# Performance work log

Measured on AMD Instinct MI355X. Metric: run time of the kernel, lower is better.

Reference implementation:

```python
import jax, jax.numpy as jnp
import numpy as np
from jax import lax

B, T, L = 128, 512, 256


def setup_inputs() -> dict:
    key = jax.random.key(0)
    k1, k2, k3 = jax.random.split(key, 3)
    labels = jax.random.randint(k1, (B, T), 0, L)
    y_true = jax.nn.one_hot(labels, L, dtype=jnp.float32)  # (B, T, L) one-hot
    y_pre = jax.random.normal(k2, (B, T, L), dtype=jnp.float32)
    trans = jax.random.normal(k3, (L, L), dtype=jnp.float32) * 0.1
    return {"y_true": y_true, "y_pre": y_pre, "trans": trans}


def reference(y_true, y_pre, trans):
    # path score: emission part + transition part
    point_score = jnp.sum(y_pre * y_true, axis=(1, 2))[:, None]  # (B, 1)
    # sum_t  one_hot(y_t)^T @ trans @ one_hot(y_{t+1})
    trans_score = jnp.einsum('btl,lm,btm->b', y_true[:, :-1], trans, y_true[:, 1:])[:, None]
    path_score = point_score + trans_score  # (B, 1)

    # forward algorithm (log-space DP) over timesteps
    def step(state, emit):
        # state: (B, L) log alpha, emit: (B, L) emissions at current step
        scores = state[:, :, None] + trans[None, :, :] + emit[:, None, :]  # (B, L, L)
        new = jax.nn.logsumexp(scores, axis=1)  # (B, L)
        return new, None

    init = y_pre[:, 0]                         # (B, L)
    emits = jnp.moveaxis(y_pre[:, 1:], 1, 0)   # (T-1, B, L)
    final, _ = lax.scan(step, init, emits)
    log_norm = jax.nn.logsumexp(final, axis=1, keepdims=True)  # (B, 1)
    return log_norm - path_score
```

## Files before the change

### kernel.cpp

```cpp
#include <hip/hip_runtime.h>
#include <hip/hip_bf16.h>

#define B_ 128
#define T_ 512
#define L_ 256

typedef float f32x4 __attribute__((ext_vector_type(4)));
typedef unsigned uint32x4 __attribute__((ext_vector_type(4)));

__device__ __forceinline__ unsigned short f2bf(float x) {
    unsigned u = __builtin_bit_cast(unsigned, x);
    return (unsigned short)((u + 0x7fff + ((u >> 16) & 1)) >> 16);
}

#define AW(n, v) asm volatile("v_accvgpr_write_b32 a" #n ", %0" :: "v"(v) : "a" #n)
#define STGF(F, A0, A1, A2, A3) { uint32x4 qq = etb4[vbase + F * 64]; \
    AW(A0, qq[0]); AW(A1, qq[1]); AW(A2, qq[2]); AW(A3, qq[3]); }

#define MFMA_AB(ACC, AF, LO, HI) \
    asm volatile("v_mfma_f32_16x16x32_bf16 %0, %1, a[" #LO ":" #HI "], %0" \
                 : "+v"(ACC) : "v"(AF))

#define BARRIER() asm volatile("s_waitcnt lgkmcnt(0)\n\ts_barrier" ::: "memory")

__global__ __launch_bounds__(256) void k_exptrans(const float* __restrict__ trans,
                                                  unsigned short* __restrict__ ETB) {
    int l = blockIdx.x;
    int m = threadIdx.x;
    unsigned short v = f2bf(__expf(trans[l * L_ + m]));
    unsigned byte = (unsigned)((m >> 4) * 8 + (l >> 5)) * 1024u
                  + (unsigned)(((l >> 3) & 3) * 16 + (m & 15)) * 16u
                  + (unsigned)(((l >> 1) & 3)) * 4u + (unsigned)(l & 1) * 2u;
    *(unsigned short*)((char*)ETB + byte) = v;
}

__global__ __launch_bounds__(256) void k_labels(const float* __restrict__ y_true,
                                                int* __restrict__ labels) {
    int wid = threadIdx.x >> 6, lane = threadIdx.x & 63;
    int r = blockIdx.x * 4 + wid;
    const float4* row = (const float4*)(y_true + (size_t)r * L_);
    float4 v = row[lane];
    int loc = -1;
    if (v.x > 0.5f) loc = lane * 4 + 0;
    if (v.y > 0.5f) loc = lane * 4 + 1;
    if (v.z > 0.5f) loc = lane * 4 + 2;
    if (v.w > 0.5f) loc = lane * 4 + 3;
    unsigned long long m = __ballot(loc >= 0);
    int src = __ffsll(m) - 1;
    int lab = __shfl(loc, src, 64);
    if (lane == 0) labels[r] = lab;
}

__global__ __launch_bounds__(256) void k_path(const float* __restrict__ y_pre,
                                              const float* __restrict__ trans,
                                              const int* __restrict__ labels,
                                              float* __restrict__ path) {
    int b = blockIdx.x, tid = threadIdx.x;
    const int* lb = labels + b * T_;
    float acc = 0.f;
    for (int t = tid; t < T_; t += 256) {
        int l1 = lb[t];
        acc += y_pre[((size_t)b * T_ + t) * L_ + l1];
        if (t + 1 < T_) acc += trans[l1 * L_ + lb[t + 1]];
    }
#pragma unroll
    for (int off = 1; off < 64; off <<= 1) acc += __shfl_xor(acc, off, 64);
    __shared__ float red[4];
    int wid = tid >> 6, lane = tid & 63;
    if (lane == 0) red[wid] = acc;
    __syncthreads();
    if (tid == 0) path[b] = red[0] + red[1] + red[2] + red[3];
}

#define MFMA32()                                                         \
        MFMA_AB(c0, af0,   0,   3); MFMA_AB(c1, af0,  32,  35);          \
        MFMA_AB(c2, af0,  64,  67); MFMA_AB(c3, af0,  96,  99);          \
        MFMA_AB(c0, af1,   4,   7); MFMA_AB(c1, af1,  36,  39);          \
        MFMA_AB(c2, af1,  68,  71); MFMA_AB(c3, af1, 100, 103);          \
        MFMA_AB(c0, af2,   8,  11); MFMA_AB(c1, af2,  40,  43);          \
        MFMA_AB(c2, af2,  72,  75); MFMA_AB(c3, af2, 104, 107);          \
        MFMA_AB(c0, af3,  12,  15); MFMA_AB(c1, af3,  44,  47);          \
        MFMA_AB(c2, af3,  76,  79); MFMA_AB(c3, af3, 108, 111);          \
        MFMA_AB(c0, af4,  16,  19); MFMA_AB(c1, af4,  48,  51);          \
        MFMA_AB(c2, af4,  80,  83); MFMA_AB(c3, af4, 112, 115);          \
        MFMA_AB(c0, af5,  20,  23); MFMA_AB(c1, af5,  52,  55);          \
        MFMA_AB(c2, af5,  84,  87); MFMA_AB(c3, af5, 116, 119);          \
        MFMA_AB(c0, af6,  24,  27); MFMA_AB(c1, af6,  56,  59);          \
        MFMA_AB(c2, af6,  88,  91); MFMA_AB(c3, af6, 120, 123);          \
        MFMA_AB(c0, af7,  28,  31); MFMA_AB(c1, af7,  60,  63);          \
        MFMA_AB(c2, af7,  92,  95); MFMA_AB(c3, af7, 124, 127);

#define STEP(TT, PH_RD, PH_WR, DSLOT, WSLOT, EREG)                       \
    {                                                                    \
        float Dt = nmr[DSLOT];               \
        float scale = __expf(NPprev + EREG - Dt);   \
        const uint32x4* pA = (const uint32x4*)ph[PH_RD];                 \
        uint32x4 af0 = pA[g];      uint32x4 af1 = pA[g + 4];             \
        uint32x4 af2 = pA[g + 8];  uint32x4 af3 = pA[g + 12];            \
        uint32x4 af4 = pA[g + 16]; uint32x4 af5 = pA[g + 20];            \
        uint32x4 af6 = pA[g + 24]; uint32x4 af7 = pA[g + 28];            \
        f32x4 c0 = {0.f,0.f,0.f,0.f}, c1 = {0.f,0.f,0.f,0.f};            \
        f32x4 c2 = {0.f,0.f,0.f,0.f}, c3 = {0.f,0.f,0.f,0.f};            \
        MFMA32()                                                         \
        float val = (g < 2) ? ((g == 0) ? c0[0] : c1[0])                 \
                            : ((g == 2) ? c2[0] : c3[0]);                \
        ph[PH_WR][st] = f2bf(val * scale);    \
        s = NPprev + __logf(val) + EREG;                 \
        if (tid == 0) nmr[WSLOT] = s;               \
        NPprev = Dt;                                                     \
        { int tp = (TT) + 4; if (tp > T_ - 1) tp = T_ - 1;               \
          EREG = yp[(size_t)tp * L_ + st]; }     \
        BARRIER();                                                       \
    }

__global__ void __launch_bounds__(256, 1)
k_forward(const float* __restrict__ yp_all,
          const unsigned short* __restrict__ ETB,
          const float* __restrict__ path,
          float* __restrict__ out) {
    int b = blockIdx.x, tid = threadIdx.x;
    int w = tid >> 6;
    int i = tid & 63;
    int g = i >> 4;
    const int st = (w << 6) + i;
    const float* yp = yp_all + (size_t)b * T_ * L_;

    {
        const uint32x4* etb4 = (const uint32x4*)ETB;
        int vbase = w * 2048 + i;
        STGF( 0,   0,  1,  2,  3)  STGF( 1,   4,  5,  6,  7)
        STGF( 2,   8,  9, 10, 11)  STGF( 3,  12, 13, 14, 15)
        STGF( 4,  16, 17, 18, 19)  STGF( 5,  20, 21, 22, 23)
        STGF( 6,  24, 25, 26, 27)  STGF( 7,  28, 29, 30, 31)
        STGF( 8,  32, 33, 34, 35)  STGF( 9,  36, 37, 38, 39)
        STGF(10,  40, 41, 42, 43)  STGF(11,  44, 45, 46, 47)
        STGF(12,  48, 49, 50, 51)  STGF(13,  52, 53, 54, 55)
        STGF(14,  56, 57, 58, 59)  STGF(15,  60, 61, 62, 63)
        STGF(16,  64, 65, 66, 67)  STGF(17,  68, 69, 70, 71)
        STGF(18,  72, 73, 74, 75)  STGF(19,  76, 77, 78, 79)
        STGF(20,  80, 81, 82, 83)  STGF(21,  84, 85, 86, 87)
        STGF(22,  88, 89, 90, 91)  STGF(23,  92, 93, 94, 95)
        STGF(24,  96, 97, 98, 99)  STGF(25, 100,101,102,103)
        STGF(26, 104,105,106,107)  STGF(27, 108,109,110,111)
        STGF(28, 112,113,114,115)  STGF(29, 116,117,118,119)
        STGF(30, 120,121,122,123)  STGF(31, 124,125,126,127)
    }

    __shared__ alignas(16) unsigned short ph[2][L_];
    __shared__ float red[8];
    __shared__ float nmr[4];

    float s = yp[st];
    {
        float v = s;
#pragma unroll
        for (int off = 1; off < 64; off <<= 1) v = fmaxf(v, __shfl_xor(v, off, 64));
        if (i == 0) red[w] = v;
        __syncthreads();
        if (tid == 0) {
            float M = fmaxf(fmaxf(red[0], red[1]), fmaxf(red[2], red[3]));
            nmr[0] = M; nmr[1] = M; nmr[2] = M; nmr[3] = M;
        }
        __syncthreads();
    }
    float NPprev = nmr[0];
    ph[1][st] = f2bf(__expf(s - NPprev));

    float e0 = yp[(size_t)1 * L_ + st];
    float e1 = yp[(size_t)2 * L_ + st];
    float e2 = yp[(size_t)3 * L_ + st];
    float e3 = yp[(size_t)4 * L_ + st];
    __syncthreads();

    for (int t = 1; t < 509; t += 4) {
        STEP(t + 0, 1, 0, 3, 1, e0)
        STEP(t + 1, 0, 1, 0, 2, e1)
        STEP(t + 2, 1, 0, 1, 3, e2)
        STEP(t + 3, 0, 1, 2, 0, e3)
    }
    STEP(509, 1, 0, 3, 1, e0)
    STEP(510, 0, 1, 0, 2, e1)
    STEP(511, 1, 0, 1, 3, e2)

    {
        float v = s;
#pragma unroll
        for (int off = 1; off < 64; off <<= 1) v = fmaxf(v, __shfl_xor(v, off, 64));
        if (i == 0) red[w] = v;
    }
    __syncthreads();
    float M = fmaxf(fmaxf(red[0], red[1]), fmaxf(red[2], red[3]));
    float e = __expf(s - M);
#pragma unroll
    for (int off = 1; off < 64; off <<= 1) e += __shfl_xor(e, off, 64);
    if (i == 0) red[4 + w] = e;
    __syncthreads();
    if (tid == 0)
        out[b] = M + __logf((red[4] + red[5]) + (red[6] + red[7])) - path[b];
}

extern "C" void kernel_launch(void* const* d_in, const int* in_sizes, int n_in,
                              void* d_out, int out_size, void* d_ws, size_t ws_size,
                              hipStream_t stream) {
    const float* y_true = (const float*)d_in[0];
    const float* y_pre  = (const float*)d_in[1];
    const float* trans  = (const float*)d_in[2];
    float* out = (float*)d_out;

    char* ws = (char*)d_ws;
    unsigned short* ETB = (unsigned short*)ws;
    int* labels = (int*)(ws + 131072);
    float* path = (float*)(ws + 131072 + 262144);

    hipLaunchKernelGGL(k_exptrans, dim3(L_), dim3(L_), 0, stream, trans, ETB);
    hipLaunchKernelGGL(k_labels, dim3(B_ * T_ / 4), dim3(256), 0, stream, y_true, labels);
    hipLaunchKernelGGL(k_path, dim3(B_), dim3(256), 0, stream, y_pre, trans, labels, path);
    hipLaunchKernelGGL(k_forward, dim3(B_), dim3(256), 0, stream, y_pre, ETB, path, out);
}
```

Measured before the change: 243.9 us.

## Process two batch sequences per block to interleave independent forward recurrences

Each forward block now runs the log-space DP for two batch elements at once. The two independent MFMA chains are interleaved so their latencies overlap, and both share one barrier and one transposed-exp(trans) register preload per step. This cuts the grid from 128 to 64 blocks, which uses fewer CUs on a 256-CU part, and doubles per-thread register and LDS work. The emission prefetch depth drops from four steps ahead to two.

```diff
diff --git a/kernel.cpp b/kernel.cpp
--- a/kernel.cpp
+++ b/kernel.cpp
@@ -72,44 +72,74 @@
     if (tid == 0) path[b] = red[0] + red[1] + red[2] + red[3];
 }
 
-#define MFMA32()                                                         \
-        MFMA_AB(c0, af0,   0,   3); MFMA_AB(c1, af0,  32,  35);          \
-        MFMA_AB(c2, af0,  64,  67); MFMA_AB(c3, af0,  96,  99);          \
-        MFMA_AB(c0, af1,   4,   7); MFMA_AB(c1, af1,  36,  39);          \
-        MFMA_AB(c2, af1,  68,  71); MFMA_AB(c3, af1, 100, 103);          \
-        MFMA_AB(c0, af2,   8,  11); MFMA_AB(c1, af2,  40,  43);          \
-        MFMA_AB(c2, af2,  72,  75); MFMA_AB(c3, af2, 104, 107);          \
-        MFMA_AB(c0, af3,  12,  15); MFMA_AB(c1, af3,  44,  47);          \
-        MFMA_AB(c2, af3,  76,  79); MFMA_AB(c3, af3, 108, 111);          \
-        MFMA_AB(c0, af4,  16,  19); MFMA_AB(c1, af4,  48,  51);          \
-        MFMA_AB(c2, af4,  80,  83); MFMA_AB(c3, af4, 112, 115);          \
-        MFMA_AB(c0, af5,  20,  23); MFMA_AB(c1, af5,  52,  55);          \
-        MFMA_AB(c2, af5,  84,  87); MFMA_AB(c3, af5, 116, 119);          \
-        MFMA_AB(c0, af6,  24,  27); MFMA_AB(c1, af6,  56,  59);          \
-        MFMA_AB(c2, af6,  88,  91); MFMA_AB(c3, af6, 120, 123);          \
-        MFMA_AB(c0, af7,  28,  31); MFMA_AB(c1, af7,  60,  63);          \
-        MFMA_AB(c2, af7,  92,  95); MFMA_AB(c3, af7, 124, 127);
-
-#define STEP(TT, PH_RD, PH_WR, DSLOT, WSLOT, EREG)                       \
+#define MFMA64()                                                         \
+    MFMA_AB(cA0, aA0,   0,   3); MFMA_AB(cB0, aB0,   0,   3);            \
+    MFMA_AB(cA1, aA0,  32,  35); MFMA_AB(cB1, aB0,  32,  35);            \
+    MFMA_AB(cA2, aA0,  64,  67); MFMA_AB(cB2, aB0,  64,  67);            \
+    MFMA_AB(cA3, aA0,  96,  99); MFMA_AB(cB3, aB0,  96,  99);            \
+    MFMA_AB(cA0, aA1,   4,   7); MFMA_AB(cB0, aB1,   4,   7);            \
+    MFMA_AB(cA1, aA1,  36,  39); MFMA_AB(cB1, aB1,  36,  39);            \
+    MFMA_AB(cA2, aA1,  68,  71); MFMA_AB(cB2, aB1,  68,  71);            \
+    MFMA_AB(cA3, aA1, 100, 103); MFMA_AB(cB3, aB1, 100, 103);            \
+    MFMA_AB(cA0, aA2,   8,  11); MFMA_AB(cB0, aB2,   8,  11);            \
+    MFMA_AB(cA1, aA2,  40,  43); MFMA_AB(cB1, aB2,  40,  43);            \
+    MFMA_AB(cA2, aA2,  72,  75); MFMA_AB(cB2, aB2,  72,  75);            \
+    MFMA_AB(cA3, aA2, 104, 107); MFMA_AB(cB3, aB2, 104, 107);            \
+    MFMA_AB(cA0, aA3,  12,  15); MFMA_AB(cB0, aB3,  12,  15);            \
+    MFMA_AB(cA1, aA3,  44,  47); MFMA_AB(cB1, aB3,  44,  47);            \
+    MFMA_AB(cA2, aA3,  76,  79); MFMA_AB(cB2, aB3,  76,  79);            \
+    MFMA_AB(cA3, aA3, 108, 111); MFMA_AB(cB3, aB3, 108, 111);            \
+    MFMA_AB(cA0, aA4,  16,  19); MFMA_AB(cB0, aB4,  16,  19);            \
+    MFMA_AB(cA1, aA4,  48,  51); MFMA_AB(cB1, aB4,  48,  51);            \
+    MFMA_AB(cA2, aA4,  80,  83); MFMA_AB(cB2, aB4,  80,  83);            \
+    MFMA_AB(cA3, aA4, 112, 115); MFMA_AB(cB3, aB4, 112, 115);            \
+    MFMA_AB(cA0, aA5,  20,  23); MFMA_AB(cB0, aB5,  20,  23);            \
+    MFMA_AB(cA1, aA5,  52,  55); MFMA_AB(cB1, aB5,  52,  55);            \
+    MFMA_AB(cA2, aA5,  84,  87); MFMA_AB(cB2, aB5,  84,  87);            \
+    MFMA_AB(cA3, aA5, 116, 119); MFMA_AB(cB3, aB5, 116, 119);            \
+    MFMA_AB(cA0, aA6,  24,  27); MFMA_AB(cB0, aB6,  24,  27);            \
+    MFMA_AB(cA1, aA6,  56,  59); MFMA_AB(cB1, aB6,  56,  59);            \
+    MFMA_AB(cA2, aA6,  88,  91); MFMA_AB(cB2, aB6,  88,  91);            \
+    MFMA_AB(cA3, aA6, 120, 123); MFMA_AB(cB3, aB6, 120, 123);            \
+    MFMA_AB(cA0, aA7,  28,  31); MFMA_AB(cB0, aB7,  28,  31);            \
+    MFMA_AB(cA1, aA7,  60,  63); MFMA_AB(cB1, aB7,  60,  63);            \
+    MFMA_AB(cA2, aA7,  92,  95); MFMA_AB(cB2, aB7,  92,  95);            \
+    MFMA_AB(cA3, aA7, 124, 127); MFMA_AB(cB3, aB7, 124, 127);
+
+#define STEPD(TT, PH_RD, PH_WR, DSLOT, WSLOT, EA, EB)                    \
     {                                                                    \
-        float Dt = nmr[DSLOT];               \
-        float scale = __expf(NPprev + EREG - Dt);   \
-        const uint32x4* pA = (const uint32x4*)ph[PH_RD];                 \
-        uint32x4 af0 = pA[g];      uint32x4 af1 = pA[g + 4];             \
-        uint32x4 af2 = pA[g + 8];  uint32x4 af3 = pA[g + 12];            \
-        uint32x4 af4 = pA[g + 16]; uint32x4 af5 = pA[g + 20];            \
-        uint32x4 af6 = pA[g + 24]; uint32x4 af7 = pA[g + 28];            \
-        f32x4 c0 = {0.f,0.f,0.f,0.f}, c1 = {0.f,0.f,0.f,0.f};            \
-        f32x4 c2 = {0.f,0.f,0.f,0.f}, c3 = {0.f,0.f,0.f,0.f};            \
-        MFMA32()                                                         \
-        float val = (g < 2) ? ((g == 0) ? c0[0] : c1[0])                 \
-                            : ((g == 2) ? c2[0] : c3[0]);                \
-        ph[PH_WR][st] = f2bf(val * scale);    \
-        s = NPprev + __logf(val) + EREG;                 \
-        if (tid == 0) nmr[WSLOT] = s;               \
-        NPprev = Dt;                                                     \
-        { int tp = (TT) + 4; if (tp > T_ - 1) tp = T_ - 1;               \
-          EREG = yp[(size_t)tp * L_ + st]; }     \
+        float eAc = EA, eBc = EB;            \
+        { int tp = (TT) + 2; if (tp > T_ - 1) tp = T_ - 1;               \
+          EA = ypA[(size_t)tp * L_ + st];                                \
+          EB = ypB[(size_t)tp * L_ + st]; }     \
+        float DtA = nmrA[DSLOT], DtB = nmrB[DSLOT];                      \
+        float scA = __expf(NPA + eAc - DtA);   \
+        float scB = __expf(NPB + eBc - DtB);                             \
+        const uint32x4* qA = (const uint32x4*)phA[PH_RD];                \
+        const uint32x4* qB = (const uint32x4*)phB[PH_RD];                \
+        uint32x4 aA0 = qA[g],      aA1 = qA[g + 4];                      \
+        uint32x4 aA2 = qA[g + 8],  aA3 = qA[g + 12];                     \
+        uint32x4 aA4 = qA[g + 16], aA5 = qA[g + 20];                     \
+        uint32x4 aA6 = qA[g + 24], aA7 = qA[g + 28];                     \
+        uint32x4 aB0 = qB[g],      aB1 = qB[g + 4];                      \
+        uint32x4 aB2 = qB[g + 8],  aB3 = qB[g + 12];                     \
+        uint32x4 aB4 = qB[g + 16], aB5 = qB[g + 20];                     \
+        uint32x4 aB6 = qB[g + 24], aB7 = qB[g + 28];                     \
+        f32x4 cA0={0.f,0.f,0.f,0.f}, cA1={0.f,0.f,0.f,0.f};              \
+        f32x4 cA2={0.f,0.f,0.f,0.f}, cA3={0.f,0.f,0.f,0.f};              \
+        f32x4 cB0={0.f,0.f,0.f,0.f}, cB1={0.f,0.f,0.f,0.f};              \
+        f32x4 cB2={0.f,0.f,0.f,0.f}, cB3={0.f,0.f,0.f,0.f};              \
+        MFMA64()                                                         \
+        float valA = (g < 2) ? ((g == 0) ? cA0[0] : cA1[0])              \
+                             : ((g == 2) ? cA2[0] : cA3[0]);             \
+        float valB = (g < 2) ? ((g == 0) ? cB0[0] : cB1[0])              \
+                             : ((g == 2) ? cB2[0] : cB3[0]);             \
+        phA[PH_WR][st] = f2bf(valA * scA);                               \
+        phB[PH_WR][st] = f2bf(valB * scB);                               \
+        sA = NPA + __logf(valA) + eAc;                   \
+        sB = NPB + __logf(valB) + eBc;                                   \
+        if (tid == 0) { nmrA[WSLOT] = sA; nmrB[WSLOT] = sB; }            \
+        NPA = DtA; NPB = DtB;                                            \
         BARRIER();                                                       \
     }
 
@@ -118,12 +148,13 @@
           const unsigned short* __restrict__ ETB,
           const float* __restrict__ path,
           float* __restrict__ out) {
-    int b = blockIdx.x, tid = threadIdx.x;
+    int blk = blockIdx.x, tid = threadIdx.x;
     int w = tid >> 6;
     int i = tid & 63;
     int g = i >> 4;
     const int st = (w << 6) + i;
-    const float* yp = yp_all + (size_t)b * T_ * L_;
+    const float* ypA = yp_all + (size_t)(2 * blk) * T_ * L_;
+    const float* ypB = ypA + (size_t)T_ * L_;
 
     {
         const uint32x4* etb4 = (const uint32x4*)ETB;
@@ -146,57 +177,79 @@
         STGF(30, 120,121,122,123)  STGF(31, 124,125,126,127)
     }
 
-    __shared__ alignas(16) unsigned short ph[2][L_];
-    __shared__ float red[8];
-    __shared__ float nmr[4];
-
-    float s = yp[st];
+    __shared__ alignas(16) unsigned short ph[2][2][L_];
+    __shared__ float red[2][8];
+    __shared__ float nmr[2][4];
+
+    unsigned short (*phA)[L_] = ph[0];
+    unsigned short (*phB)[L_] = ph[1];
+    float* nmrA = nmr[0];
+    float* nmrB = nmr[1];
+
+    float sA = ypA[st], sB = ypB[st];
     {
-        float v = s;
+        float v = sA;
 #pragma unroll
         for (int off = 1; off < 64; off <<= 1) v = fmaxf(v, __shfl_xor(v, off, 64));
-        if (i == 0) red[w] = v;
+        if (i == 0) red[0][w] = v;
+        float u = sB;
+#pragma unroll
+        for (int off = 1; off < 64; off <<= 1) u = fmaxf(u, __shfl_xor(u, off, 64));
+        if (i == 0) red[1][w] = u;
         __syncthreads();
         if (tid == 0) {
-            float M = fmaxf(fmaxf(red[0], red[1]), fmaxf(red[2], red[3]));
-            nmr[0] = M; nmr[1] = M; nmr[2] = M; nmr[3] = M;
+            float MA = fmaxf(fmaxf(red[0][0], red[0][1]), fmaxf(red[0][2], red[0][3]));
+            float MB = fmaxf(fmaxf(red[1][0], red[1][1]), fmaxf(red[1][2], red[1][3]));
+            nmrA[0] = MA; nmrA[1] = MA; nmrA[2] = MA; nmrA[3] = MA;
+            nmrB[0] = MB; nmrB[1] = MB; nmrB[2] = MB; nmrB[3] = MB;
         }
         __syncthreads();
     }
-    float NPprev = nmr[0];
-    ph[1][st] = f2bf(__expf(s - NPprev));
-
-    float e0 = yp[(size_t)1 * L_ + st];
-    float e1 = yp[(size_t)2 * L_ + st];
-    float e2 = yp[(size_t)3 * L_ + st];
-    float e3 = yp[(size_t)4 * L_ + st];
+    float NPA = nmrA[0], NPB = nmrB[0];
+    phA[1][st] = f2bf(__expf(sA - NPA));
+    phB[1][st] = f2bf(__expf(sB - NPB));
+
+    float eXA = ypA[(size_t)1 * L_ + st], eYA = ypA[(size_t)2 * L_ + st];
+    float eXB = ypB[(size_t)1 * L_ + st], eYB = ypB[(size_t)2 * L_ + st];
     __syncthreads();
 
     for (int t = 1; t < 509; t += 4) {
-        STEP(t + 0, 1, 0, 3, 1, e0)
-        STEP(t + 1, 0, 1, 0, 2, e1)
-        STEP(t + 2, 1, 0, 1, 3, e2)
-        STEP(t + 3, 0, 1, 2, 0, e3)
-    }
-    STEP(509, 1, 0, 3, 1, e0)
-    STEP(510, 0, 1, 0, 2, e1)
-    STEP(511, 1, 0, 1, 3, e2)
+        STEPD(t + 0, 1, 0, 3, 1, eXA, eXB)
+        STEPD(t + 1, 0, 1, 0, 2, eYA, eYB)
+        STEPD(t + 2, 1, 0, 1, 3, eXA, eXB)
+        STEPD(t + 3, 0, 1, 2, 0, eYA, eYB)
+    }
+    STEPD(509, 1, 0, 3, 1, eXA, eXB)
+    STEPD(510, 0, 1, 0, 2, eYA, eYB)
+    STEPD(511, 1, 0, 1, 3, eXA, eXB)
 
     {
-        float v = s;
+        float v = sA;
 #pragma unroll
         for (int off = 1; off < 64; off <<= 1) v = fmaxf(v, __shfl_xor(v, off, 64));
-        if (i == 0) red[w] = v;
-    }
-    __syncthreads();
-    float M = fmaxf(fmaxf(red[0], red[1]), fmaxf(red[2], red[3]));
-    float e = __expf(s - M);
-#pragma unroll
-    for (int off = 1; off < 64; off <<= 1) e += __shfl_xor(e, off, 64);
-    if (i == 0) red[4 + w] = e;
-    __syncthreads();
-    if (tid == 0)
-        out[b] = M + __logf((red[4] + red[5]) + (red[6] + red[7])) - path[b];
+        if (i == 0) red[0][w] = v;
+        float u = sB;
+#pragma unroll
+        for (int off = 1; off < 64; off <<= 1) u = fmaxf(u, __shfl_xor(u, off, 64));
+        if (i == 0) red[1][w] = u;
+    }
+    __syncthreads();
+    float MA = fmaxf(fmaxf(red[0][0], red[0][1]), fmaxf(red[0][2], red[0][3]));
+    float MB = fmaxf(fmaxf(red[1][0], red[1][1]), fmaxf(red[1][2], red[1][3]));
+    float eA = __expf(sA - MA);
+    float eB = __expf(sB - MB);
+#pragma unroll
+    for (int off = 1; off < 64; off <<= 1) eA += __shfl_xor(eA, off, 64);
+#pragma unroll
+    for (int off = 1; off < 64; off <<= 1) eB += __shfl_xor(eB, off, 64);
+    if (i == 0) { red[0][4 + w] = eA; red[1][4 + w] = eB; }
+    __syncthreads();
+    if (tid == 0) {
+        out[2 * blk]     = MA + __logf((red[0][4] + red[0][5]) + (red[0][6] + red[0][7]))
+                           - path[2 * blk];
+        out[2 * blk + 1] = MB + __logf((red[1][4] + red[1][5]) + (red[1][6] + red[1][7]))
+                           - path[2 * blk + 1];
+    }
 }
 
 extern "C" void kernel_launch(void* const* d_in, const int* in_sizes, int n_in,
@@ -215,5 +268,5 @@
     hipLaunchKernelGGL(k_exptrans, dim3(L_), dim3(L_), 0, stream, trans, ETB);
     hipLaunchKernelGGL(k_labels, dim3(B_ * T_ / 4), dim3(256), 0, stream, y_true, labels);
     hipLaunchKernelGGL(k_path, dim3(B_), dim3(256), 0, stream, y_pre, trans, labels, path);
-    hipLaunchKernelGGL(k_forward, dim3(B_), dim3(256), 0, stream, y_pre, ETB, path, out);
-}
+    hipLaunchKernelGGL(k_forward, dim3(B_ / 2), dim3(256), 0, stream, y_pre, ETB, path, out);
+}
```

Result: slower. 419.3 us (+71.9%).
